# Optimization experiments

Measured on AMD Instinct MI355X. Metric: run time of the kernel, lower is better.

The kernel has to match this reference:

```python
import jax, jax.numpy as jnp
import numpy as np

B, IN, OUT = 1024, 512, 64000
EPS = 1e-12  # matches torch F.normalize eps


def setup_inputs() -> dict:
    key = jax.random.key(0)
    k1, k2, k3 = jax.random.split(key, 3)
    x = jax.random.normal(k1, (B, IN), dtype=jnp.float32)
    label = jax.random.randint(k2, (B,), 0, OUT)
    # xavier_uniform_ for weight [OUT, IN]: limit = sqrt(6 / (fan_in + fan_out))
    limit = float(np.sqrt(6.0 / (IN + OUT)))
    weight = jax.random.uniform(k3, (OUT, IN), dtype=jnp.float32, minval=-limit, maxval=limit)
    s = 50               # python scalar; set via _calculate_para but UNUSED in normfree output
    m = jnp.full((1,), 0.5, dtype=jnp.float32)  # margin
    return {"x": x, "label": label, "weight": weight, "s": s, "m": m}


def reference(x, label, weight, s, m):
    m = m.reshape(())
    cos_m, sin_m = jnp.cos(m), jnp.sin(m)
    # norm of raw input (the 'normfree' scale replacing s)
    norm = jnp.linalg.norm(x, axis=1, keepdims=True)            # [B, 1]
    xn = x / jnp.maximum(norm, EPS)                             # F.normalize(input)
    wn = weight / jnp.maximum(
        jnp.linalg.norm(weight, axis=1, keepdims=True), EPS)    # F.normalize(weight)
    cosine = xn @ wn.T                                          # [B, OUT]
    sine = jnp.sqrt(jnp.clip(1.0 - cosine * cosine, 0.0, None))
    phi = cosine * cos_m - sine * sin_m                         # cos(theta + m)
    # per-sample loop in torch == one-hot substitution only where cosine > 0
    onehot = jax.nn.one_hot(label, OUT, dtype=bool)             # [B, OUT]
    mod_cosine = jnp.where(onehot & (cosine > 0), phi, cosine)
    return norm * mod_cosine, wn
```

## Files before the change

### kernel.cpp

```cpp
#include <hip/hip_runtime.h>
#include <cstdint>

#define EPSN 1e-12f
static constexpr int B_ROWS = 1024;
static constexpr int IN_DIM = 512;
static constexpr int OUT_DIM = 64000;

typedef __attribute__((ext_vector_type(8))) short bf16x8;
typedef __attribute__((ext_vector_type(4))) float f32x4;

__device__ __forceinline__ unsigned short f2bf(float f) {
  uint32_t u = __builtin_bit_cast(uint32_t, f);
  u += 0x7fffu + ((u >> 16) & 1u);
  return (unsigned short)(u >> 16);
}

__device__ __forceinline__ float bf2f(unsigned short h) {
  uint32_t u = (uint32_t)h << 16;
  return __builtin_bit_cast(float, u);
}

__device__ __forceinline__ float wave_sum(float v) {
#pragma unroll
  for (int off = 32; off; off >>= 1) v += __shfl_xor(v, off);
  return v;
}

__device__ __forceinline__ void async16(const void* g, void* l) {
  __builtin_amdgcn_global_load_lds((const __attribute__((address_space(1))) uint32_t*)g,
                                   (__attribute__((address_space(3))) uint32_t*)l, 16, 0, 0);
}

__global__ void prep_kernel(const float* __restrict__ X, const int* __restrict__ label,
                            const float* __restrict__ Wg, float* __restrict__ norms,
                            float* __restrict__ fixdot, unsigned short* __restrict__ xbf) {
  int lane = threadIdx.x & 63;
  int row = blockIdx.x * 4 + (threadIdx.x >> 6);
  const float* src = X + (size_t)row * IN_DIM + lane * 8;
  float4 a = *(const float4*)src;
  float4 b = *(const float4*)(src + 4);
  uint4 u;
  u.x = (uint32_t)f2bf(a.x) | ((uint32_t)f2bf(a.y) << 16);
  u.y = (uint32_t)f2bf(a.z) | ((uint32_t)f2bf(a.w) << 16);
  u.z = (uint32_t)f2bf(b.x) | ((uint32_t)f2bf(b.y) << 16);
  u.w = (uint32_t)f2bf(b.z) | ((uint32_t)f2bf(b.w) << 16);
  *(uint4*)(xbf + (size_t)row * IN_DIM + lane * 8) = u;
  float ssx = a.x * a.x;
  ssx = fmaf(a.y, a.y, ssx); ssx = fmaf(a.z, a.z, ssx); ssx = fmaf(a.w, a.w, ssx);
  ssx = fmaf(b.x, b.x, ssx); ssx = fmaf(b.y, b.y, ssx); ssx = fmaf(b.z, b.z, ssx);
  ssx = fmaf(b.w, b.w, ssx);
  int lab = label[row];
  const float* wsrc = Wg + (size_t)lab * IN_DIM + lane * 8;
  float4 wa = *(const float4*)wsrc, wb = *(const float4*)(wsrc + 4);
  float d = a.x * wa.x;
  d = fmaf(a.y, wa.y, d); d = fmaf(a.z, wa.z, d); d = fmaf(a.w, wa.w, d);
  d = fmaf(b.x, wb.x, d); d = fmaf(b.y, wb.y, d); d = fmaf(b.z, wb.z, d);
  d = fmaf(b.w, wb.w, d);
  float ssw = wa.x * wa.x;
  ssw = fmaf(wa.y, wa.y, ssw); ssw = fmaf(wa.z, wa.z, ssw); ssw = fmaf(wa.w, wa.w, ssw);
  ssw = fmaf(wb.x, wb.x, ssw); ssw = fmaf(wb.y, wb.y, ssw); ssw = fmaf(wb.z, wb.z, ssw);
  ssw = fmaf(wb.w, wb.w, ssw);
  ssx = wave_sum(ssx);
  d = wave_sum(d);
  ssw = wave_sum(ssw);
  if (lane == 0) {
    norms[row] = sqrtf(ssx);
    fixdot[row] = d / fmaxf(sqrtf(ssw), EPSN);
  }
}

__global__ void wcast_kernel(const float* __restrict__ Wg, unsigned short* __restrict__ wbf) {
  int lane = threadIdx.x & 63;
  int row = blockIdx.x * 4 + (threadIdx.x >> 6);
  const float* src = Wg + (size_t)row * IN_DIM + lane * 8;
  float4 a = *(const float4*)src;
  float4 b = *(const float4*)(src + 4);
  float ss = a.x * a.x;
  ss = fmaf(a.y, a.y, ss); ss = fmaf(a.z, a.z, ss); ss = fmaf(a.w, a.w, ss);
  ss = fmaf(b.x, b.x, ss); ss = fmaf(b.y, b.y, ss); ss = fmaf(b.z, b.z, ss);
  ss = fmaf(b.w, b.w, ss);
  ss = wave_sum(ss);
  float inv = 1.0f / fmaxf(sqrtf(ss), EPSN);
  uint4 u;
  u.x = (uint32_t)f2bf(a.x * inv) | ((uint32_t)f2bf(a.y * inv) << 16);
  u.y = (uint32_t)f2bf(a.z * inv) | ((uint32_t)f2bf(a.w * inv) << 16);
  u.z = (uint32_t)f2bf(b.x * inv) | ((uint32_t)f2bf(b.y * inv) << 16);
  u.w = (uint32_t)f2bf(b.z * inv) | ((uint32_t)f2bf(b.w * inv) << 16);
  *(uint4*)(wbf + (size_t)row * IN_DIM + lane * 8) = u;
}

__global__ __launch_bounds__(512, 2) void gemm_epi_kernel(
    const unsigned short* __restrict__ Abf, const unsigned short* __restrict__ Bbf,
    const float* __restrict__ norms, const float* __restrict__ fixdot,
    const int* __restrict__ label, const float* __restrict__ mArr,
    float* __restrict__ out0, float* __restrict__ wnOut) {
  __shared__ char smem[131072];

  const int t = threadIdx.x;
  int flat = blockIdx.x;
  int xcd = flat & 7;
  int wk = (flat >> 3) + xcd * 125;
  int mT = wk & 3, nT = wk >> 2;
  int rowA0 = mT * 256, rowB0 = nT * 256;

  int lane = t & 63;
  int wid = t >> 6;
  int wm = wid >> 2, wn2 = wid & 3;
  int rl = lane & 15, sl = lane >> 4;

  int r0 = t >> 2, q0 = (t & 3) ^ ((r0 >> 1) & 3);
  int r1 = (t + 512) >> 2, q1 = ((t + 512) & 3) ^ ((r1 >> 1) & 3);
  const unsigned short* aP0 = Abf + (size_t)(rowA0 + r0) * IN_DIM + q0 * 8;
  const unsigned short* aP1 = Abf + (size_t)(rowA0 + r1) * IN_DIM + q1 * 8;
  const unsigned short* bP0 = Bbf + (size_t)(rowB0 + r0) * IN_DIM + q0 * 8;
  const unsigned short* bP1 = Bbf + (size_t)(rowB0 + r1) * IN_DIM + q1 * 8;

  auto issueSub = [&](int sig) {
    int kcol = sig * 32;
    char* aD = smem + (sig & 3) * 16384;
    char* bD = smem + 65536 + (sig & 3) * 16384;
    async16(aP0 + kcol, aD + t * 16);
    async16(aP1 + kcol, aD + (t + 512) * 16);
    async16(bP0 + kcol, bD + t * 16);
    async16(bP1 + kcol, bD + (t + 512) * 16);
  };

  issueSub(0); issueSub(1); issueSub(2);

  f32x4 acc[8][4];
#pragma unroll
  for (int m = 0; m < 8; ++m)
#pragma unroll
    for (int n = 0; n < 4; ++n) acc[m][n] = (f32x4){0.f, 0.f, 0.f, 0.f};

#pragma unroll 1
  for (int sigma = 0; sigma < 16; ++sigma) {
    __builtin_amdgcn_sched_barrier(0);
    if (sigma <= 13)      asm volatile("s_waitcnt vmcnt(8)" ::: "memory");
    else if (sigma == 14) asm volatile("s_waitcnt vmcnt(4)" ::: "memory");
    else                  asm volatile("s_waitcnt vmcnt(0)" ::: "memory");
    __builtin_amdgcn_s_barrier();
    __builtin_amdgcn_sched_barrier(0);
    if (sigma + 3 <= 15) issueSub(sigma + 3);

    const char* aB = smem + (sigma & 3) * 16384;
    const char* bB = smem + 65536 + (sigma & 3) * 16384;
    bf16x8 av[8], bv[4];
#pragma unroll
    for (int m = 0; m < 8; ++m) {
      int r = wm * 128 + m * 16 + rl;
      av[m] = *(const bf16x8*)(aB + r * 64 + ((sl ^ ((r >> 1) & 3)) * 16));
    }
#pragma unroll
    for (int n = 0; n < 4; ++n) {
      int r = wn2 * 64 + n * 16 + rl;
      bv[n] = *(const bf16x8*)(bB + r * 64 + ((sl ^ ((r >> 1) & 3)) * 16));
    }
    __builtin_amdgcn_s_setprio(1);
#pragma unroll
    for (int n = 0; n < 4; ++n)
#pragma unroll
      for (int m = 0; m < 8; ++m)
        acc[m][n] = __builtin_amdgcn_mfma_f32_16x16x32_bf16(av[m], bv[n], acc[m][n], 0, 0, 0);
    __builtin_amdgcn_s_setprio(0);
  }

  {
    int r = t >> 3;
    int c0 = (t & 7) * 64;
    int row = rowB0 + mT * 64 + r;
    const unsigned short* srcp = Bbf + (size_t)row * IN_DIM + c0;
    float* dst = wnOut + (size_t)row * IN_DIM + c0;
#pragma unroll
    for (int g = 0; g < 8; ++g) {
      uint4 uu = *(const uint4*)(srcp + g * 8);
      float4 f;
      f.x = bf2f((unsigned short)(uu.x & 0xffff)); f.y = bf2f((unsigned short)(uu.x >> 16));
      f.z = bf2f((unsigned short)(uu.y & 0xffff)); f.w = bf2f((unsigned short)(uu.y >> 16));
      *(float4*)(dst + g * 8) = f;
      f.x = bf2f((unsigned short)(uu.z & 0xffff)); f.y = bf2f((unsigned short)(uu.z >> 16));
      f.z = bf2f((unsigned short)(uu.w & 0xffff)); f.w = bf2f((unsigned short)(uu.w >> 16));
      *(float4*)(dst + g * 8 + 4) = f;
    }
  }

  float mm = mArr[0];
  float cm = cosf(mm), sm = sinf(mm);
  int rowb = rowA0 + wm * 128, colb = rowB0 + wn2 * 64;
#pragma unroll
  for (int m = 0; m < 8; ++m) {
#pragma unroll
    for (int q = 0; q < 4; ++q) {
      int R = rowb + m * 16 + sl * 4 + q;
      int lab = label[R];
      float nv = norms[R], fv = fixdot[R];
      float* orow = out0 + (size_t)R * OUT_DIM;
#pragma unroll
      for (int n = 0; n < 4; ++n) {
        int Cc = colb + n * 16 + rl;
        float val = acc[m][n][q];
        if (Cc == lab) {
          float c = fv / fmaxf(nv, EPSN);
          val = (c > 0.f) ? nv * (c * cm - sqrtf(fmaxf(1.f - c * c, 0.f)) * sm) : fv;
        }
        orow[Cc] = val;
      }
    }
  }
}

extern "C" void kernel_launch(void* const* d_in, const int* in_sizes, int n_in,
                              void* d_out, int out_size, void* d_ws, size_t ws_size,
                              hipStream_t stream) {
  const float* x = (const float*)d_in[0];
  const int* label = (const int*)d_in[1];
  const float* weight = (const float*)d_in[2];
  const float* mArr = (const float*)d_in[4];

  float* out0 = (float*)d_out;
  float* wnOut = out0 + (size_t)B_ROWS * OUT_DIM;

  char* ws = (char*)d_ws;
  float* norms = (float*)ws;
  float* fixdot = (float*)(ws + 4096);
  unsigned short* xbf = (unsigned short*)(ws + 8192);
  unsigned short* wbf = (unsigned short*)(ws + 8192 + 2ull * B_ROWS * IN_DIM);

  prep_kernel<<<B_ROWS / 4, 256, 0, stream>>>(x, label, weight, norms, fixdot, xbf);
  wcast_kernel<<<OUT_DIM / 4, 256, 0, stream>>>(weight, wbf);
  gemm_epi_kernel<<<1000, 512, 0, stream>>>(xbf, wbf, norms, fixdot, label, mArr,
                                            out0, wnOut);
}
```

Baseline: 209.1 us.

## Shrink GEMM tile to 256x128 with 4 waves and 3-stage LDS ring

The fused GEMM+epilogue kernel moves from 256x256 tiles with 8 waves and a 4-deep LDS pipeline (128KB) to 256x128 tiles with 4 waves and a 3-slot ring buffer (72KB), launching 2000 blocks instead of 1000. Each wave keeps the same 128x64 accumulator footprint. The aim is a smaller LDS footprint and finer grid granularity, so more blocks can be resident per CU and the last wave of blocks balances better. In exchange, A-tile reuse per B byte halves, raising L2 traffic for the bf16 activations, and the prefetch distance drops from three stages to two.

```diff
diff --git a/kernel.cpp b/kernel.cpp
--- a/kernel.cpp
+++ b/kernel.cpp
@@ -89,43 +89,51 @@
   *(uint4*)(wbf + (size_t)row * IN_DIM + lane * 8) = u;
 }
 
-__global__ __launch_bounds__(512, 2) void gemm_epi_kernel(
+__global__ __launch_bounds__(256, 2) void gemm_epi_kernel(
     const unsigned short* __restrict__ Abf, const unsigned short* __restrict__ Bbf,
     const float* __restrict__ norms, const float* __restrict__ fixdot,
     const int* __restrict__ label, const float* __restrict__ mArr,
     float* __restrict__ out0, float* __restrict__ wnOut) {
-  __shared__ char smem[131072];
+  __shared__ char smem[73728];
 
   const int t = threadIdx.x;
   int flat = blockIdx.x;
   int xcd = flat & 7;
-  int wk = (flat >> 3) + xcd * 125;
+  int wk = (flat >> 3) + xcd * 250;
   int mT = wk & 3, nT = wk >> 2;
-  int rowA0 = mT * 256, rowB0 = nT * 256;
+  int rowA0 = mT * 256, rowB0 = nT * 128;
 
   int lane = t & 63;
   int wid = t >> 6;
-  int wm = wid >> 2, wn2 = wid & 3;
+  int wm = wid >> 1, wn2 = wid & 1;
   int rl = lane & 15, sl = lane >> 4;
 
-  int r0 = t >> 2, q0 = (t & 3) ^ ((r0 >> 1) & 3);
-  int r1 = (t + 512) >> 2, q1 = ((t + 512) & 3) ^ ((r1 >> 1) & 3);
-  const unsigned short* aP0 = Abf + (size_t)(rowA0 + r0) * IN_DIM + q0 * 8;
-  const unsigned short* aP1 = Abf + (size_t)(rowA0 + r1) * IN_DIM + q1 * 8;
-  const unsigned short* bP0 = Bbf + (size_t)(rowB0 + r0) * IN_DIM + q0 * 8;
-  const unsigned short* bP1 = Bbf + (size_t)(rowB0 + r1) * IN_DIM + q1 * 8;
-
-  auto issueSub = [&](int sig) {
+  const unsigned short* aP[4];
+  const unsigned short* bP[2];
+#pragma unroll
+  for (int c = 0; c < 4; ++c) {
+    int ch = t + c * 256;
+    int r = ch >> 2, q = (ch & 3) ^ ((r >> 1) & 3);
+    aP[c] = Abf + (size_t)(rowA0 + r) * IN_DIM + q * 8;
+  }
+#pragma unroll
+  for (int c = 0; c < 2; ++c) {
+    int ch = t + c * 256;
+    int r = ch >> 2, q = (ch & 3) ^ ((r >> 1) & 3);
+    bP[c] = Bbf + (size_t)(rowB0 + r) * IN_DIM + q * 8;
+  }
+
+  auto issueSub = [&](int sig, int slot) {
     int kcol = sig * 32;
-    char* aD = smem + (sig & 3) * 16384;
-    char* bD = smem + 65536 + (sig & 3) * 16384;
-    async16(aP0 + kcol, aD + t * 16);
-    async16(aP1 + kcol, aD + (t + 512) * 16);
-    async16(bP0 + kcol, bD + t * 16);
-    async16(bP1 + kcol, bD + (t + 512) * 16);
+    char* aD = smem + slot * 24576;
+    char* bD = aD + 16384;
+#pragma unroll
+    for (int c = 0; c < 4; ++c) async16(aP[c] + kcol, aD + (t + c * 256) * 16);
+#pragma unroll
+    for (int c = 0; c < 2; ++c) async16(bP[c] + kcol, bD + (t + c * 256) * 16);
   };
 
-  issueSub(0); issueSub(1); issueSub(2);
+  issueSub(0, 0); issueSub(1, 1);
 
   f32x4 acc[8][4];
 #pragma unroll
@@ -133,18 +141,18 @@
 #pragma unroll
     for (int n = 0; n < 4; ++n) acc[m][n] = (f32x4){0.f, 0.f, 0.f, 0.f};
 
+  int slotR = 0, slotW = 2;
 #pragma unroll 1
   for (int sigma = 0; sigma < 16; ++sigma) {
     __builtin_amdgcn_sched_barrier(0);
-    if (sigma <= 13)      asm volatile("s_waitcnt vmcnt(8)" ::: "memory");
-    else if (sigma == 14) asm volatile("s_waitcnt vmcnt(4)" ::: "memory");
-    else                  asm volatile("s_waitcnt vmcnt(0)" ::: "memory");
+    if (sigma <= 14) asm volatile("s_waitcnt vmcnt(6)" ::: "memory");
+    else             asm volatile("s_waitcnt vmcnt(0)" ::: "memory");
     __builtin_amdgcn_s_barrier();
     __builtin_amdgcn_sched_barrier(0);
-    if (sigma + 3 <= 15) issueSub(sigma + 3);
-
-    const char* aB = smem + (sigma & 3) * 16384;
-    const char* bB = smem + 65536 + (sigma & 3) * 16384;
+    if (sigma <= 13) issueSub(sigma + 2, slotW);
+
+    const char* aB = smem + slotR * 24576;
+    const char* bB = aB + 16384;
     bf16x8 av[8], bv[4];
 #pragma unroll
     for (int m = 0; m < 8; ++m) {
@@ -163,12 +171,14 @@
       for (int m = 0; m < 8; ++m)
         acc[m][n] = __builtin_amdgcn_mfma_f32_16x16x32_bf16(av[m], bv[n], acc[m][n], 0, 0, 0);
     __builtin_amdgcn_s_setprio(0);
+    slotR = (slotR == 2) ? 0 : slotR + 1;
+    slotW = (slotW == 2) ? 0 : slotW + 1;
   }
 
   {
     int r = t >> 3;
     int c0 = (t & 7) * 64;
-    int row = rowB0 + mT * 64 + r;
+    int row = rowB0 + mT * 32 + r;
     const unsigned short* srcp = Bbf + (size_t)row * IN_DIM + c0;
     float* dst = wnOut + (size_t)row * IN_DIM + c0;
 #pragma unroll
@@ -228,6 +238,6 @@
 
   prep_kernel<<<B_ROWS / 4, 256, 0, stream>>>(x, label, weight, norms, fixdot, xbf);
   wcast_kernel<<<OUT_DIM / 4, 256, 0, stream>>>(weight, wbf);
-  gemm_epi_kernel<<<1000, 512, 0, stream>>>(xbf, wbf, norms, fixdot, label, mArr,
+  gemm_epi_kernel<<<2000, 256, 0, stream>>>(xbf, wbf, norms, fixdot, label, mArr,
                                             out0, wnOut);
 }
```

New measurement: 214.2 us. 1.02x slower.

## Fuse weight normalization and bf16 cast into GEMM, keep full-K B tile in LDS

Applied to the files above, without the earlier changes.

Removes the separate weight-cast kernel. Each GEMM block now loads its 128 weight rows in fp32, normalizes them, and stores them as bf16 in a swizzled full-K LDS tile. Only the x tiles are streamed, double-buffered. The block tile shrinks to 256x128 with 2000 blocks, and wnOut is written from LDS. This avoids the bf16 weight round trip through global memory and one kernel launch. In exchange, each weight tile is read and normalized 4 times (once per M tile), LDS use grows to 160KB (likely one block per CU), and the prologue is not overlapped with the GEMM.

```diff
diff --git a/kernel.cpp b/kernel.cpp
--- a/kernel.cpp
+++ b/kernel.cpp
@@ -69,126 +69,122 @@
   }
 }
 
-__global__ void wcast_kernel(const float* __restrict__ Wg, unsigned short* __restrict__ wbf) {
-  int lane = threadIdx.x & 63;
-  int row = blockIdx.x * 4 + (threadIdx.x >> 6);
-  const float* src = Wg + (size_t)row * IN_DIM + lane * 8;
-  float4 a = *(const float4*)src;
-  float4 b = *(const float4*)(src + 4);
-  float ss = a.x * a.x;
-  ss = fmaf(a.y, a.y, ss); ss = fmaf(a.z, a.z, ss); ss = fmaf(a.w, a.w, ss);
-  ss = fmaf(b.x, b.x, ss); ss = fmaf(b.y, b.y, ss); ss = fmaf(b.z, b.z, ss);
-  ss = fmaf(b.w, b.w, ss);
-  ss = wave_sum(ss);
-  float inv = 1.0f / fmaxf(sqrtf(ss), EPSN);
-  uint4 u;
-  u.x = (uint32_t)f2bf(a.x * inv) | ((uint32_t)f2bf(a.y * inv) << 16);
-  u.y = (uint32_t)f2bf(a.z * inv) | ((uint32_t)f2bf(a.w * inv) << 16);
-  u.z = (uint32_t)f2bf(b.x * inv) | ((uint32_t)f2bf(b.y * inv) << 16);
-  u.w = (uint32_t)f2bf(b.z * inv) | ((uint32_t)f2bf(b.w * inv) << 16);
-  *(uint4*)(wbf + (size_t)row * IN_DIM + lane * 8) = u;
-}
-
-__global__ __launch_bounds__(512, 2) void gemm_epi_kernel(
-    const unsigned short* __restrict__ Abf, const unsigned short* __restrict__ Bbf,
+__global__ __launch_bounds__(512, 2) void gemm_fused_kernel(
+    const float* __restrict__ Wg, const unsigned short* __restrict__ Abf,
     const float* __restrict__ norms, const float* __restrict__ fixdot,
     const int* __restrict__ label, const float* __restrict__ mArr,
     float* __restrict__ out0, float* __restrict__ wnOut) {
-  __shared__ char smem[131072];
+  __shared__ char smem[163840];
 
   const int t = threadIdx.x;
   int flat = blockIdx.x;
   int xcd = flat & 7;
-  int wk = (flat >> 3) + xcd * 125;
+  int wk = (flat >> 3) + xcd * 250;
   int mT = wk & 3, nT = wk >> 2;
-  int rowA0 = mT * 256, rowB0 = nT * 256;
+  int rowA0 = mT * 256, rowB0 = nT * 128;
 
   int lane = t & 63;
   int wid = t >> 6;
-  int wm = wid >> 2, wn2 = wid & 3;
+  int wm = wid >> 1, wn2 = wid & 1;
   int rl = lane & 15, sl = lane >> 4;
 
-  int r0 = t >> 2, q0 = (t & 3) ^ ((r0 >> 1) & 3);
-  int r1 = (t + 512) >> 2, q1 = ((t + 512) & 3) ^ ((r1 >> 1) & 3);
-  const unsigned short* aP0 = Abf + (size_t)(rowA0 + r0) * IN_DIM + q0 * 8;
-  const unsigned short* aP1 = Abf + (size_t)(rowA0 + r1) * IN_DIM + q1 * 8;
-  const unsigned short* bP0 = Bbf + (size_t)(rowB0 + r0) * IN_DIM + q0 * 8;
-  const unsigned short* bP1 = Bbf + (size_t)(rowB0 + r1) * IN_DIM + q1 * 8;
-
-  auto issueSub = [&](int sig) {
+#pragma unroll 1
+  for (int rr = 0; rr < 16; ++rr) {
+    int r = wid * 16 + rr;
+    const float* src = Wg + (size_t)(rowB0 + r) * IN_DIM + lane * 8;
+    float4 a = *(const float4*)src;
+    float4 b = *(const float4*)(src + 4);
+    float ss = a.x * a.x;
+    ss = fmaf(a.y, a.y, ss); ss = fmaf(a.z, a.z, ss); ss = fmaf(a.w, a.w, ss);
+    ss = fmaf(b.x, b.x, ss); ss = fmaf(b.y, b.y, ss); ss = fmaf(b.z, b.z, ss);
+    ss = fmaf(b.w, b.w, ss);
+    ss = wave_sum(ss);
+    float inv = 1.0f / fmaxf(sqrtf(ss), EPSN);
+    uint4 u;
+    u.x = (uint32_t)f2bf(a.x * inv) | ((uint32_t)f2bf(a.y * inv) << 16);
+    u.y = (uint32_t)f2bf(a.z * inv) | ((uint32_t)f2bf(a.w * inv) << 16);
+    u.z = (uint32_t)f2bf(b.x * inv) | ((uint32_t)f2bf(b.y * inv) << 16);
+    u.w = (uint32_t)f2bf(b.z * inv) | ((uint32_t)f2bf(b.w * inv) << 16);
+    *(uint4*)(smem + r * 1024 + ((lane ^ (r & 7)) * 16)) = u;
+  }
+  __syncthreads();
+
+  int rA0 = t >> 2, qA0 = (t & 3) ^ ((rA0 >> 1) & 3);
+  int rA1 = (t + 512) >> 2, qA1 = ((t + 512) & 3) ^ ((rA1 >> 1) & 3);
+  const unsigned short* aP0 = Abf + (size_t)(rowA0 + rA0) * IN_DIM + qA0 * 8;
+  const unsigned short* aP1 = Abf + (size_t)(rowA0 + rA1) * IN_DIM + qA1 * 8;
+
+  auto issueA = [&](int sig) {
+    char* aD = smem + 131072 + (sig & 1) * 16384;
     int kcol = sig * 32;
-    char* aD = smem + (sig & 3) * 16384;
-    char* bD = smem + 65536 + (sig & 3) * 16384;
     async16(aP0 + kcol, aD + t * 16);
     async16(aP1 + kcol, aD + (t + 512) * 16);
-    async16(bP0 + kcol, bD + t * 16);
-    async16(bP1 + kcol, bD + (t + 512) * 16);
   };
 
-  issueSub(0); issueSub(1); issueSub(2);
-
-  f32x4 acc[8][4];
-#pragma unroll
-  for (int m = 0; m < 8; ++m)
+  issueA(0); issueA(1);
+
+  f32x4 acc[4][4];
+#pragma unroll
+  for (int m = 0; m < 4; ++m)
 #pragma unroll
     for (int n = 0; n < 4; ++n) acc[m][n] = (f32x4){0.f, 0.f, 0.f, 0.f};
 
 #pragma unroll 1
   for (int sigma = 0; sigma < 16; ++sigma) {
     __builtin_amdgcn_sched_barrier(0);
-    if (sigma <= 13)      asm volatile("s_waitcnt vmcnt(8)" ::: "memory");
-    else if (sigma == 14) asm volatile("s_waitcnt vmcnt(4)" ::: "memory");
-    else                  asm volatile("s_waitcnt vmcnt(0)" ::: "memory");
+    if (sigma <= 14) asm volatile("s_waitcnt vmcnt(2)" ::: "memory");
+    else             asm volatile("s_waitcnt vmcnt(0)" ::: "memory");
     __builtin_amdgcn_s_barrier();
     __builtin_amdgcn_sched_barrier(0);
-    if (sigma + 3 <= 15) issueSub(sigma + 3);
-
-    const char* aB = smem + (sigma & 3) * 16384;
-    const char* bB = smem + 65536 + (sigma & 3) * 16384;
-    bf16x8 av[8], bv[4];
-#pragma unroll
-    for (int m = 0; m < 8; ++m) {
-      int r = wm * 128 + m * 16 + rl;
+
+    const char* aB = smem + 131072 + (sigma & 1) * 16384;
+    bf16x8 av[4], bv[4];
+#pragma unroll
+    for (int m = 0; m < 4; ++m) {
+      int r = wm * 64 + m * 16 + rl;
       av[m] = *(const bf16x8*)(aB + r * 64 + ((sl ^ ((r >> 1) & 3)) * 16));
     }
 #pragma unroll
     for (int n = 0; n < 4; ++n) {
       int r = wn2 * 64 + n * 16 + rl;
-      bv[n] = *(const bf16x8*)(bB + r * 64 + ((sl ^ ((r >> 1) & 3)) * 16));
+      bv[n] = *(const bf16x8*)(smem + r * 1024 + (((sigma * 4 + sl) ^ (r & 7)) * 16));
     }
     __builtin_amdgcn_s_setprio(1);
 #pragma unroll
     for (int n = 0; n < 4; ++n)
 #pragma unroll
-      for (int m = 0; m < 8; ++m)
+      for (int m = 0; m < 4; ++m)
         acc[m][n] = __builtin_amdgcn_mfma_f32_16x16x32_bf16(av[m], bv[n], acc[m][n], 0, 0, 0);
     __builtin_amdgcn_s_setprio(0);
+    asm volatile("s_waitcnt lgkmcnt(0)" ::: "memory");
+    __builtin_amdgcn_s_barrier();
+    __builtin_amdgcn_sched_barrier(0);
+    if (sigma + 2 <= 15) issueA(sigma + 2);
   }
 
   {
-    int r = t >> 3;
-    int c0 = (t & 7) * 64;
-    int row = rowB0 + mT * 64 + r;
-    const unsigned short* srcp = Bbf + (size_t)row * IN_DIM + c0;
-    float* dst = wnOut + (size_t)row * IN_DIM + c0;
-#pragma unroll
-    for (int g = 0; g < 8; ++g) {
-      uint4 uu = *(const uint4*)(srcp + g * 8);
+    int r = mT * 32 + (t >> 4);
+    int row = rowB0 + r;
+    float* dst = wnOut + (size_t)row * IN_DIM + (t & 15) * 32;
+#pragma unroll
+    for (int j = 0; j < 4; ++j) {
+      int s = (t & 15) * 4 + j;
+      uint4 uu = *(const uint4*)(smem + r * 1024 + ((s ^ (r & 7)) * 16));
       float4 f;
       f.x = bf2f((unsigned short)(uu.x & 0xffff)); f.y = bf2f((unsigned short)(uu.x >> 16));
       f.z = bf2f((unsigned short)(uu.y & 0xffff)); f.w = bf2f((unsigned short)(uu.y >> 16));
-      *(float4*)(dst + g * 8) = f;
+      *(float4*)(dst + j * 8) = f;
       f.x = bf2f((unsigned short)(uu.z & 0xffff)); f.y = bf2f((unsigned short)(uu.z >> 16));
       f.z = bf2f((unsigned short)(uu.w & 0xffff)); f.w = bf2f((unsigned short)(uu.w >> 16));
-      *(float4*)(dst + g * 8 + 4) = f;
+      *(float4*)(dst + j * 8 + 4) = f;
     }
   }
 
   float mm = mArr[0];
   float cm = cosf(mm), sm = sinf(mm);
-  int rowb = rowA0 + wm * 128, colb = rowB0 + wn2 * 64;
-#pragma unroll
-  for (int m = 0; m < 8; ++m) {
+  int rowb = rowA0 + wm * 64, colb = rowB0 + wn2 * 64;
+#pragma unroll
+  for (int m = 0; m < 4; ++m) {
 #pragma unroll
     for (int q = 0; q < 4; ++q) {
       int R = rowb + m * 16 + sl * 4 + q;
@@ -224,10 +220,8 @@
   float* norms = (float*)ws;
   float* fixdot = (float*)(ws + 4096);
   unsigned short* xbf = (unsigned short*)(ws + 8192);
-  unsigned short* wbf = (unsigned short*)(ws + 8192 + 2ull * B_ROWS * IN_DIM);
 
   prep_kernel<<<B_ROWS / 4, 256, 0, stream>>>(x, label, weight, norms, fixdot, xbf);
-  wcast_kernel<<<OUT_DIM / 4, 256, 0, stream>>>(weight, wbf);
-  gemm_epi_kernel<<<1000, 512, 0, stream>>>(xbf, wbf, norms, fixdot, label, mArr,
-                                            out0, wnOut);
-}
+  gemm_fused_kernel<<<2000, 512, 0, stream>>>(weight, xbf, norms, fixdot, label,
+                                              mArr, out0, wnOut);
+}
```

Result: slower. 278.8 us (+33.4%).
